# Performance work log

Measured on AMD Instinct MI355X. Metric: run time of the kernel, lower is better.

## Reference

```python
import jax, jax.numpy as jnp
import numpy as np

EMBED = 192
EXPAND = 3
D1 = EMBED * EXPAND  # 576
RPE_IN = 32
LAYERS = 3
LAMBDA = 0.95


def _rpe_mlp(t, w0, b0, ws, bs, wo, bo):
    # t: (2n, 1) relative positions -> (2n, D1) Toeplitz coefficients
    h = t @ w0.T + b0
    for i in range(ws.shape[0]):
        h = jax.nn.relu(h) @ ws[i].T + bs[i]
    return jax.nn.relu(h) @ wo.T + bo


def _toeplitz(x, a):
    # Toeplitz matmul via length-2n circular convolution (FFT).
    # x: (B, n, d); a: (2n, d) coeffs ordered [t0, t1..t_{n-1}, pad, neg half]
    n = x.shape[1]
    m = 2 * n
    xf = jnp.fft.rfft(x, m, axis=1)
    af = jnp.fft.rfft(a, m, axis=0)
    return jnp.fft.irfft(xf * af[None], m, axis=1)[:, :n]


def _forward(x, p_w, p_b, q_w, q_b, v_w, v_b, o_w, o_b, slope,
             t1_w0, t1_b0, t1_ws, t1_bs, t1_wo, t1_bo,
             t2_w0, t2_b0, t2_ws, t2_bs, t2_wo, t2_bo):
    b, h, w, d = x.shape
    n = h  # square grid: h == w, rpe/decay built from n = x.shape[1]
    dt = x.dtype

    pos = jnp.arange(1, n, dtype=dt).reshape(-1, 1)          # (n-1, 1)
    zero = jnp.zeros((1, 1), dt)
    rpe_input = jnp.concatenate([zero, pos, zero, -pos], axis=0)  # (2n, 1)

    p = jax.nn.silu(x @ p_w.T + p_b)
    q = jax.nn.silu(x @ q_w.T + q_b)
    v = jax.nn.silu(x @ v_w.T + v_b)

    # decay mask: slope clamped to [0,1], blended with lambda, powered by |lag|
    sl = LAMBDA + (1.0 - LAMBDA) * jnp.clip(slope, 0.0, 1.0)  # (1, D1)
    idx = jnp.arange(1, n, dtype=dt).reshape(1, -1, 1)        # (1, n-1, 1)
    gamma = sl ** idx                                          # (1, n-1, D1)
    one = jnp.ones((1, 1, D1), dt)
    decay = jnp.concatenate([one, gamma, one, gamma[:, ::-1]], axis=1)[0]  # (2n, D1)

    a1 = _rpe_mlp(rpe_input, t1_w0, t1_b0, t1_ws, t1_bs, t1_wo, t1_bo) * decay
    a2 = _rpe_mlp(rpe_input, t2_w0, t2_b0, t2_ws, t2_bs, t2_wo, t2_bo) * decay

    qv = q * v                                                 # (b, h, w, D1)
    # axial mixing: tno1 along width, tno2 along height
    o1 = _toeplitz(qv.reshape(b * h, w, D1), a1).reshape(b, h, w, D1)
    o2 = _toeplitz(jnp.transpose(qv, (0, 2, 1, 3)).reshape(b * w, h, D1), a2)
    o2 = jnp.transpose(o2.reshape(b, w, h, D1), (0, 2, 1, 3))
    out = p * (o1 + o2)
    return out @ o_w.T + o_b


def setup_inputs() -> dict:
    key = jax.random.key(0)
    ks = jax.random.split(key, 8)

    def lin(k, out_d, in_d):
        k1, k2 = jax.random.split(k)
        s = 1.0 / np.sqrt(in_d)
        return (jax.random.uniform(k1, (out_d, in_d), jnp.float32, -s, s),
                jax.random.uniform(k2, (out_d,), jnp.float32, -s, s))

    x = jax.random.normal(ks[0], (8, 56, 56, EMBED), jnp.float32)
    p_w, p_b = lin(ks[1], D1, EMBED)
    q_w, q_b = lin(ks[2], D1, EMBED)
    v_w, v_b = lin(ks[3], D1, EMBED)
    o_w, o_b = lin(ks[4], EMBED, D1)
    # slope init: 1/arange(1, d1+1)^(1/(index+1)), index=0
    slope = (1.0 / jnp.arange(1, D1 + 1, dtype=jnp.float32)).reshape(1, -1)

    def tno_params(kb):
        kk = jax.random.split(kb, 2 + LAYERS)
        w0, b0 = lin(kk[0], RPE_IN, 1)
        ws, bs = [], []
        for i in range(LAYERS):
            wi, bi = lin(kk[1 + i], RPE_IN, RPE_IN)
            ws.append(wi); bs.append(bi)
        wo, bo = lin(kk[1 + LAYERS], D1, RPE_IN)
        return w0, b0, jnp.stack(ws), jnp.stack(bs), wo, bo

    t1 = tno_params(ks[5])
    t2 = tno_params(ks[6])
    return {"x": x, "p_w": p_w, "p_b": p_b, "q_w": q_w, "q_b": q_b,
            "v_w": v_w, "v_b": v_b, "o_w": o_w, "o_b": o_b, "slope": slope,
            "t1_w0": t1[0], "t1_b0": t1[1], "t1_ws": t1[2], "t1_bs": t1[3], "t1_wo": t1[4], "t1_bo": t1[5],
            "t2_w0": t2[0], "t2_b0": t2[1], "t2_ws": t2[2], "t2_bs": t2[3], "t2_wo": t2[4], "t2_bo": t2[5]}


def reference(x, p_w, p_b, q_w, q_b, v_w, v_b, o_w, o_b, slope,
              t1_w0, t1_b0, t1_ws, t1_bs, t1_wo, t1_bo,
              t2_w0, t2_b0, t2_ws, t2_bs, t2_wo, t2_bo):
    return _forward(x, p_w, p_b, q_w, q_b, v_w, v_b, o_w, o_b, slope,
                    t1_w0, t1_b0, t1_ws, t1_bs, t1_wo, t1_bo,
                    t2_w0, t2_b0, t2_ws, t2_bs, t2_wo, t2_bo)
```

## Files before the change

### kernel.cpp

```cpp
#include <hip/hip_runtime.h>
#include <hip/hip_bf16.h>
#include <math.h>

typedef unsigned short u16;
typedef short bf16x8 __attribute__((ext_vector_type(8)));
typedef float f32x4 __attribute__((ext_vector_type(4)));

#define NB 8
#define NN 56
#define M2 112
#define EMB 192
#define D1 576
#define TOK (NB*NN*NN)

__device__ __forceinline__ float bf2f(unsigned int u) {
    union { unsigned int i; float f; } v; v.i = u << 16; return v.f;
}
__device__ __forceinline__ u16 f2bf(float f) {
    union { float f; unsigned int i; } v; v.f = f;
    unsigned int x = v.i;
    return (u16)((x + 0x7fffu + ((x >> 16) & 1u)) >> 16);
}
__device__ __forceinline__ float fast_silu(float x) {
    float e = __builtin_amdgcn_exp2f(-1.442695041f * x);
    return x * __builtin_amdgcn_rcpf(1.0f + e);
}
__device__ __forceinline__ void async16(void* lds, const void* g) {
    __builtin_amdgcn_global_load_lds(
        (const __attribute__((address_space(1))) void*)g,
        (__attribute__((address_space(3))) void*)lds, 16, 0, 0);
}

#define XCH (TOK*EMB/4)
#define WCH (D1*EMB/4)
__global__ __launch_bounds__(256) void convert_kernel(
    const float* __restrict__ x,
    const float* __restrict__ pw, const float* __restrict__ qw,
    const float* __restrict__ vw, const float* __restrict__ ow,
    u16* __restrict__ xb, u16* __restrict__ wb, u16* __restrict__ owb)
{
    int tid = blockIdx.x * 256 + threadIdx.x;
    const float* src; u16* dst; int off;
    if (tid < XCH) { src = x; dst = xb; off = tid; }
    else {
        int r = tid - XCH;
        int seg = r / WCH; off = r % WCH;
        if (seg == 0)      { src = pw; dst = wb; }
        else if (seg == 1) { src = qw; dst = wb + D1*EMB; }
        else if (seg == 2) { src = vw; dst = wb + 2*D1*EMB; }
        else if (seg == 3) { src = ow; dst = owb; }
        else return;
    }
    float4 f = *(const float4*)(src + off * 4);
    ushort4 o;
    o.x = f2bf(f.x); o.y = f2bf(f.y); o.z = f2bf(f.z); o.w = f2bf(f.w);
    *(ushort4*)(dst + off * 4) = o;
}

__global__ __launch_bounds__(576) void rpe_kernel(
    const float* __restrict__ slope,
    const float* w0a, const float* b0a, const float* wsa, const float* bsa,
    const float* woa, const float* boa,
    const float* w0b, const float* b0b, const float* wsb, const float* bsb,
    const float* wob, const float* bob,
    float* __restrict__ A1, float* __restrict__ A2)
{
    int wq  = blockIdx.x / M2;
    int row = blockIdx.x % M2;
    const float* w0 = wq ? w0b : w0a;  const float* b0 = wq ? b0b : b0a;
    const float* ws = wq ? wsb : wsa;  const float* bs = wq ? bsb : bsa;
    const float* wo = wq ? wob : woa;  const float* bo = wq ? bob : boa;
    float* A = wq ? A2 : A1;

    float tval = (row == 0 || row == 56) ? 0.0f
               : (row < 56 ? (float)row : -(float)(row - 56));
    int kexp = (row == 0 || row == 56) ? 0 : (row < 56 ? row : 112 - row);

    __shared__ float h[32], g[32];
    int t = threadIdx.x;
    if (t < 32) h[t] = tval * w0[t] + b0[t];
    __syncthreads();
    for (int L = 0; L < 3; L++) {
        if (t < 32) g[t] = fmaxf(h[t], 0.0f);
        __syncthreads();
        float hn = 0.0f;
        if (t < 32) {
            hn = bs[L * 32 + t];
            for (int k = 0; k < 32; k++)
                hn = fmaf(g[k], ws[(L * 32 + t) * 32 + k], hn);
        }
        __syncthreads();
        if (t < 32) h[t] = hn;
        __syncthreads();
    }
    if (t < 32) g[t] = fmaxf(h[t], 0.0f);
    __syncthreads();

    float o = bo[t];
    for (int k = 0; k < 32; k++)
        o = fmaf(g[k], wo[t * 32 + k], o);

    float sl = slope[t];
    sl = 0.95f + 0.05f * fminf(fmaxf(sl, 0.0f), 1.0f);
    float dec = powf(sl, (float)kexp);
    A[row * D1 + t] = o * dec;
}

__global__ __launch_bounds__(256) void tbuild_kernel(
    const float* __restrict__ A1, const float* __restrict__ A2,
    u16* __restrict__ T1t, u16* __restrict__ T2t)
{
    int d = blockIdx.x;
    const float* src = blockIdx.y ? A2 : A1;
    u16* dst = blockIdx.y ? T2t : T1t;
    __shared__ float win[111];
    int t = threadIdx.x;
    if (t < 111) {
        int lag = t - 55;
        int rowi = lag + (lag < 0 ? 112 : 0);
        win[t] = src[rowi * D1 + d];
    }
    __syncthreads();
    int i = t >> 2, jq = (t & 3) * 16;
    u16 vals[16];
    #pragma unroll
    for (int jj = 0; jj < 16; jj++) {
        int j = jq + jj;
        float v = (i < 56 && j < 56) ? win[i - j + 55] : 0.0f;
        vals[jj] = f2bf(v);
    }
    u16* out = dst + ((size_t)d * 64 + i) * 64 + jq;
    *(uint4*)(out)     = *(uint4*)&vals[0];
    *(uint4*)(out + 8) = *(uint4*)&vals[8];
}

__global__ __launch_bounds__(512, 4) void proj_kernel(
    const u16* __restrict__ xb, const u16* __restrict__ wb,
    const float* __restrict__ pb, const float* __restrict__ qb,
    const float* __restrict__ vb,
    u16* __restrict__ P_T, u16* __restrict__ QV_T)
{
    __shared__ u16 lds[40960];
    int m0 = blockIdx.x * 128, n0 = blockIdx.y * 64;
    int t = threadIdx.x;
    int l = t & 63, wave = t >> 6;
    int wm = wave >> 2, wn = wave & 3;
    int col16 = l & 15, q = l >> 4;

    f32x4 accp[4], accq[4], accv[4];
    #pragma unroll
    for (int i = 0; i < 4; i++) {
        accp[i] = (f32x4){0,0,0,0};
        accq[i] = (f32x4){0,0,0,0};
        accv[i] = (f32x4){0,0,0,0};
    }

    auto stage = [&](int kc, int buf) {
        int bo = buf * 20480;
        #pragma unroll
        for (int ii = 0; ii < 2; ii++) {
            int slot = ii * 512 + t;
            int r = slot >> 3, s = slot & 7;
            int g = s ^ (r & 7);
            async16(&lds[bo + slot * 8], xb + (m0 + r) * EMB + kc * 64 + g * 8);
        }
        #pragma unroll
        for (int ii = 0; ii < 3; ii++) {
            int slot = ii * 512 + t;
            int mat = slot >> 9, cc = slot & 511;
            int r = cc >> 3, s = cc & 7;
            int g = s ^ (r & 7);
            async16(&lds[bo + 8192 + slot * 8],
                    wb + mat * (D1 * EMB) + (n0 + r) * EMB + kc * 64 + g * 8);
        }
    };

    auto compute = [&](int bo) {
        #pragma unroll
        for (int kk = 0; kk < 2; kk++) {
            int sw = ((q + 4 * kk) ^ (col16 & 7)) * 8;
            bf16x8 af[4];
            #pragma unroll
            for (int mt = 0; mt < 4; mt++)
                af[mt] = *(const bf16x8*)&lds[bo + (wm * 64 + mt * 16 + col16) * 64 + sw];
            bf16x8 bfr[3];
            #pragma unroll
            for (int mat = 0; mat < 3; mat++)
                bfr[mat] = *(const bf16x8*)&lds[bo + 8192 + mat * 4096 + (wn * 16 + col16) * 64 + sw];
            #pragma unroll
            for (int mt = 0; mt < 4; mt++) {
                accp[mt] = __builtin_amdgcn_mfma_f32_16x16x32_bf16(af[mt], bfr[0], accp[mt], 0, 0, 0);
                accq[mt] = __builtin_amdgcn_mfma_f32_16x16x32_bf16(af[mt], bfr[1], accq[mt], 0, 0, 0);
                accv[mt] = __builtin_amdgcn_mfma_f32_16x16x32_bf16(af[mt], bfr[2], accv[mt], 0, 0, 0);
            }
        }
    };

    stage(0, 0);
    stage(1, 1);
    asm volatile("s_waitcnt vmcnt(5)" ::: "memory");
    __builtin_amdgcn_s_barrier();
    compute(0);
    __builtin_amdgcn_s_barrier();
    stage(2, 0);
    asm volatile("s_waitcnt vmcnt(5)" ::: "memory");
    __builtin_amdgcn_s_barrier();
    compute(20480);
    asm volatile("s_waitcnt vmcnt(0)" ::: "memory");
    __builtin_amdgcn_s_barrier();
    compute(0);

    int n = n0 + wn * 16 + col16;
    float pbv = pb[n], qbv = qb[n], vbv = vb[n];
    size_t drow = (size_t)n * TOK + m0 + wm * 64;
    #pragma unroll
    for (int mt = 0; mt < 4; mt++) {
        ushort4 o;
        o.x = f2bf(fast_silu(accp[mt][0] + pbv));
        o.y = f2bf(fast_silu(accp[mt][1] + pbv));
        o.z = f2bf(fast_silu(accp[mt][2] + pbv));
        o.w = f2bf(fast_silu(accp[mt][3] + pbv));
        *(ushort4*)&P_T[drow + mt * 16 + q * 4] = o;
    }
    #pragma unroll
    for (int mt = 0; mt < 4; mt++) {
        ushort4 o;
        o.x = f2bf(fast_silu(accq[mt][0] + qbv) * fast_silu(accv[mt][0] + vbv));
        o.y = f2bf(fast_silu(accq[mt][1] + qbv) * fast_silu(accv[mt][1] + vbv));
        o.z = f2bf(fast_silu(accq[mt][2] + qbv) * fast_silu(accv[mt][2] + vbv));
        o.w = f2bf(fast_silu(accq[mt][3] + qbv) * fast_silu(accv[mt][3] + vbv));
        *(ushort4*)&QV_T[drow + mt * 16 + q * 4] = o;
    }
}

__global__ __launch_bounds__(256) void tno_mfma(
    const u16* __restrict__ QV_T, const u16* __restrict__ T1t,
    const u16* __restrict__ T2t, const u16* __restrict__ P_T,
    u16* __restrict__ U_T)
{
    __shared__ u16 T1s[4096];
    __shared__ u16 T2s[4096];
    __shared__ u16 Qn[64 * 72];
    __shared__ u16 Qt[64 * 72];
    __shared__ float O1f[56 * 68];
    int d = blockIdx.x, b = blockIdx.y;
    int t = threadIdx.x;
    size_t base = (size_t)d * TOK + (size_t)b * 3136;

    #pragma unroll
    for (int k = 0; k < 2; k++) {
        int slot = t + k * 256;
        int i = slot >> 3, s = slot & 7;
        int g = s ^ (i & 7);
        async16(&T1s[slot * 8], T1t + ((size_t)d * 64 + i) * 64 + g * 8);
        async16(&T2s[slot * 8], T2t + ((size_t)d * 64 + i) * 64 + g * 8);
    }
    for (int c = t; c < 392; c += 256) {
        int h = c / 7, w8 = (c % 7) * 8;
        uint4 v = *(const uint4*)(QV_T + base + c * 8);
        *(uint4*)&Qn[h * 72 + w8] = v;
        u16 e[8];
        *(uint4*)e = v;
        #pragma unroll
        for (int k = 0; k < 8; k++)
            Qt[(w8 + k) * 72 + h] = e[k];
    }
    if (t < 56) {
        uint4 z = {0, 0, 0, 0};
        *(uint4*)&Qn[t * 72 + 56] = z;
        *(uint4*)&Qt[t * 72 + 56] = z;
    }
    __syncthreads();

    int l = t & 63, wave = t >> 6;
    int col16 = l & 15, q = l >> 4;

    f32x4 acc1[4], acc2[4];
    #pragma unroll
    for (int i = 0; i < 4; i++) { acc1[i] = (f32x4){0,0,0,0}; acc2[i] = (f32x4){0,0,0,0}; }

    #pragma unroll
    for (int kk = 0; kk < 2; kk++) {
        int sw = ((q + 4 * kk) ^ (col16 & 7)) * 8;
        bf16x8 bq1 = *(const bf16x8*)&Qn[(wave * 16 + col16) * 72 + kk * 32 + q * 8];
        bf16x8 bq2 = *(const bf16x8*)&Qt[(wave * 16 + col16) * 72 + kk * 32 + q * 8];
        #pragma unroll
        for (int mt = 0; mt < 4; mt++) {
            bf16x8 a1 = *(const bf16x8*)&T1s[(mt * 16 + col16) * 64 + sw];
            bf16x8 a2 = *(const bf16x8*)&T2s[(mt * 16 + col16) * 64 + sw];
            acc1[mt] = __builtin_amdgcn_mfma_f32_16x16x32_bf16(a1, bq1, acc1[mt], 0, 0, 0);
            acc2[mt] = __builtin_amdgcn_mfma_f32_16x16x32_bf16(a2, bq2, acc2[mt], 0, 0, 0);
        }
    }

    {
        int n = wave * 16 + col16;
        if (n < 56) {
            #pragma unroll
            for (int mt = 0; mt < 4; mt++)
                #pragma unroll
                for (int r = 0; r < 4; r++) {
                    int m = mt * 16 + q * 4 + r;
                    if (m < 56) O1f[n * 68 + m] = acc1[mt][r];
                }
        }
    }
    __syncthreads();
    {
        int n = wave * 16 + col16;
        if (n < 56) {
            #pragma unroll
            for (int mt = 0; mt < 4; mt++)
                #pragma unroll
                for (int r = 0; r < 4; r++) {
                    int m = mt * 16 + q * 4 + r;
                    if (m < 56) O1f[m * 68 + n] += acc2[mt][r];
                }
        }
    }
    __syncthreads();
    for (int c = t; c < 392; c += 256) {
        int h = c / 7, w8 = (c % 7) * 8;
        f32x4 s0 = *(const f32x4*)&O1f[h * 68 + w8];
        f32x4 s1 = *(const f32x4*)&O1f[h * 68 + w8 + 4];
        uint4 pv = *(const uint4*)(P_T + base + c * 8);
        u16 pe[8];
        *(uint4*)pe = pv;
        u16 ue[8];
        #pragma unroll
        for (int k = 0; k < 4; k++) ue[k] = f2bf(bf2f(pe[k]) * s0[k]);
        #pragma unroll
        for (int k = 0; k < 4; k++) ue[4 + k] = f2bf(bf2f(pe[4 + k]) * s1[k]);
        *(uint4*)(U_T + base + c * 8) = *(uint4*)ue;
    }
}

__global__ __launch_bounds__(256) void outproj_kernel(
    const u16* __restrict__ U_T, const u16* __restrict__ owb,
    const float* __restrict__ ob, float* __restrict__ out)
{
    __shared__ char ldsraw[40960];
    u16* Uscr = (u16*)ldsraw;
    u16* As   = (u16*)(ldsraw + 16384);
    u16* Bs   = (u16*)(ldsraw + 32768);
    int m0 = blockIdx.x * 128, n0 = blockIdx.y * 64;
    int t = threadIdx.x;
    int l = t & 63, wave = t >> 6;
    int wm = wave >> 1, wn = wave & 1;
    int col16 = l & 15, q = l >> 4;

    f32x4 acc[4][2];
    #pragma unroll
    for (int i = 0; i < 4; i++)
        #pragma unroll
        for (int j = 0; j < 2; j++) acc[i][j] = (f32x4){0,0,0,0};

    for (int k0 = 0; k0 < 9; k0++) {
        #pragma unroll
        for (int ii = 0; ii < 4; ii++) {
            int slot = ii * 256 + t;
            int dd = slot >> 4, tk = slot & 15;
            async16(&Uscr[slot * 8],
                    U_T + (size_t)(k0 * 64 + dd) * TOK + m0 + tk * 8);
        }
        #pragma unroll
        for (int ii = 0; ii < 2; ii++) {
            int slot = ii * 256 + t;
            int r = slot >> 3, s = slot & 7;
            int g = s ^ (r & 7);
            async16(&Bs[slot * 8], owb + (n0 + r) * D1 + k0 * 64 + g * 8);
        }
        asm volatile("s_waitcnt vmcnt(2)" ::: "memory");
        __builtin_amdgcn_s_barrier();
        #pragma unroll
        for (int ii = 0; ii < 4; ii++) {
            int c = ii * 256 + t;
            int tok = c & 127, dc = c >> 7;
            u16 e[8];
            #pragma unroll
            for (int j = 0; j < 8; j++)
                e[j] = Uscr[(dc * 8 + j) * 128 + tok];
            int s = dc ^ (tok & 7);
            *(uint4*)&As[tok * 64 + s * 8] = *(uint4*)e;
        }
        __syncthreads();

        #pragma unroll
        for (int kk = 0; kk < 2; kk++) {
            int sw = ((q + 4 * kk) ^ (col16 & 7)) * 8;
            bf16x8 af[4];
            #pragma unroll
            for (int mt = 0; mt < 4; mt++)
                af[mt] = *(const bf16x8*)&As[(wm * 64 + mt * 16 + col16) * 64 + sw];
            bf16x8 bfr[2];
            #pragma unroll
            for (int nt = 0; nt < 2; nt++)
                bfr[nt] = *(const bf16x8*)&Bs[(wn * 32 + nt * 16 + col16) * 64 + sw];
            #pragma unroll
            for (int mt = 0; mt < 4; mt++)
                #pragma unroll
                for (int nt = 0; nt < 2; nt++)
                    acc[mt][nt] = __builtin_amdgcn_mfma_f32_16x16x32_bf16(
                        af[mt], bfr[nt], acc[mt][nt], 0, 0, 0);
        }
        __syncthreads();
    }

    float* scr = (float*)ldsraw + wave * 2304;
    float obv[2];
    #pragma unroll
    for (int nt = 0; nt < 2; nt++)
        obv[nt] = ob[n0 + wn * 32 + nt * 16 + col16];
    #pragma unroll
    for (int mt = 0; mt < 4; mt++)
        #pragma unroll
        for (int nt = 0; nt < 2; nt++)
            #pragma unroll
            for (int r = 0; r < 4; r++)
                scr[(mt * 16 + q * 4 + r) * 36 + nt * 16 + col16] =
                    acc[mt][nt][r] + obv[nt];
    __syncthreads();
    #pragma unroll
    for (int k = 0; k < 8; k++) {
        int row = k * 8 + (l >> 3), cs = (l & 7) * 4;
        f32x4 v = *(const f32x4*)&scr[row * 36 + cs];
        *(f32x4*)&out[(m0 + wm * 64 + row) * EMB + n0 + wn * 32 + cs] = v;
    }
}

extern "C" void kernel_launch(void* const* d_in, const int* in_sizes, int n_in,
                              void* d_out, int out_size, void* d_ws, size_t ws_size,
                              hipStream_t stream)
{
    (void)in_sizes; (void)n_in; (void)out_size; (void)ws_size;
    const float* x     = (const float*)d_in[0];
    const float* p_w   = (const float*)d_in[1];
    const float* p_b   = (const float*)d_in[2];
    const float* q_w   = (const float*)d_in[3];
    const float* q_b   = (const float*)d_in[4];
    const float* v_w   = (const float*)d_in[5];
    const float* v_b   = (const float*)d_in[6];
    const float* o_w   = (const float*)d_in[7];
    const float* o_b   = (const float*)d_in[8];
    const float* slope = (const float*)d_in[9];
    const float* t1_w0 = (const float*)d_in[10];
    const float* t1_b0 = (const float*)d_in[11];
    const float* t1_ws = (const float*)d_in[12];
    const float* t1_bs = (const float*)d_in[13];
    const float* t1_wo = (const float*)d_in[14];
    const float* t1_bo = (const float*)d_in[15];
    const float* t2_w0 = (const float*)d_in[16];
    const float* t2_b0 = (const float*)d_in[17];
    const float* t2_ws = (const float*)d_in[18];
    const float* t2_bs = (const float*)d_in[19];
    const float* t2_wo = (const float*)d_in[20];
    const float* t2_bo = (const float*)d_in[21];

    char* ws = (char*)d_ws;
    float* A1  = (float*)ws;
    float* A2  = (float*)(ws + 258048);
    u16*   PT  = (u16*)(ws + 516096);
    u16*   QVT = (u16*)(ws + 29417472);
    u16*   UT  = (u16*)(ws + 58318848);
    u16*   xb  = (u16*)(ws + 87220224);
    u16*   wb  = (u16*)(ws + 96854016);
    u16*   owb = (u16*)(ws + 97517568);
    u16*   T1t = (u16*)(ws + 97738752);
    u16*   T2t = (u16*)(ws + 102457344);

    convert_kernel<<<(XCH + 4*WCH + 255) / 256, 256, 0, stream>>>(
        x, p_w, q_w, v_w, o_w, xb, wb, owb);
    rpe_kernel<<<224, 576, 0, stream>>>(slope,
        t1_w0, t1_b0, t1_ws, t1_bs, t1_wo, t1_bo,
        t2_w0, t2_b0, t2_ws, t2_bs, t2_wo, t2_bo, A1, A2);
    tbuild_kernel<<<dim3(576, 2), 256, 0, stream>>>(A1, A2, T1t, T2t);
    proj_kernel<<<dim3(TOK / 128, D1 / 64), 512, 0, stream>>>(
        xb, wb, p_b, q_b, v_b, PT, QVT);
    tno_mfma<<<dim3(D1, NB), 256, 0, stream>>>(QVT, T1t, T2t, PT, UT);
    outproj_kernel<<<dim3(TOK / 128, EMB / 64), 256, 0, stream>>>(
        UT, owb, o_b, (float*)d_out);
}
```

Before: 200.8 us.

## Enlarge proj GEMM M tile to 256 and drop LDS double buffering

The projection kernel now covers 256 tokens per block instead of 128. Each wave computes a 64x32 output tile (2 N sub-tiles) instead of 64x16, so every A fragment read from LDS feeds more MFMAs. The two-buffer async pipeline is replaced with a single buffer that is loaded, waited on, and computed for each k-chunk. This cuts LDS footprint and redundant B loads, but it removes the overlap of loads with compute, doubles accumulator registers (which may limit occupancy under launch_bounds 512,4), and halves the grid size.

```diff
diff --git a/kernel.cpp b/kernel.cpp
--- a/kernel.cpp
+++ b/kernel.cpp
@@ -140,96 +140,101 @@
     const float* __restrict__ vb,
     u16* __restrict__ P_T, u16* __restrict__ QV_T)
 {
-    __shared__ u16 lds[40960];
-    int m0 = blockIdx.x * 128, n0 = blockIdx.y * 64;
+    __shared__ u16 lds[28672];
+    u16* As = lds;
+    u16* Bs = lds + 16384;
+    int m0 = blockIdx.x * 256, n0 = blockIdx.y * 64;
     int t = threadIdx.x;
     int l = t & 63, wave = t >> 6;
-    int wm = wave >> 2, wn = wave & 3;
+    int wg = wave >> 1, wn = wave & 1;
     int col16 = l & 15, q = l >> 4;
 
-    f32x4 accp[4], accq[4], accv[4];
-    #pragma unroll
-    for (int i = 0; i < 4; i++) {
-        accp[i] = (f32x4){0,0,0,0};
-        accq[i] = (f32x4){0,0,0,0};
-        accv[i] = (f32x4){0,0,0,0};
-    }
-
-    auto stage = [&](int kc, int buf) {
-        int bo = buf * 20480;
-        #pragma unroll
-        for (int ii = 0; ii < 2; ii++) {
-            int slot = ii * 512 + t;
-            int r = slot >> 3, s = slot & 7;
+    f32x4 accp[4][2], accq[4][2], accv[4][2];
+    #pragma unroll
+    for (int i = 0; i < 4; i++)
+        #pragma unroll
+        for (int j = 0; j < 2; j++) {
+            accp[i][j] = (f32x4){0,0,0,0};
+            accq[i][j] = (f32x4){0,0,0,0};
+            accv[i][j] = (f32x4){0,0,0,0};
+        }
+
+    auto stage = [&](int kc) {
+        #pragma unroll
+        for (int ii = 0; ii < 4; ii++) {
+            int c = ii * 512 + t;
+            int r = c >> 3, s = c & 7;
             int g = s ^ (r & 7);
-            async16(&lds[bo + slot * 8], xb + (m0 + r) * EMB + kc * 64 + g * 8);
+            async16(&As[c * 8], xb + (m0 + r) * EMB + kc * 64 + g * 8);
         }
         #pragma unroll
         for (int ii = 0; ii < 3; ii++) {
-            int slot = ii * 512 + t;
-            int mat = slot >> 9, cc = slot & 511;
+            int c = ii * 512 + t;
+            int mat = c >> 9, cc = c & 511;
             int r = cc >> 3, s = cc & 7;
             int g = s ^ (r & 7);
-            async16(&lds[bo + 8192 + slot * 8],
+            async16(&Bs[c * 8],
                     wb + mat * (D1 * EMB) + (n0 + r) * EMB + kc * 64 + g * 8);
         }
     };
 
-    auto compute = [&](int bo) {
+    #pragma unroll
+    for (int kc = 0; kc < 3; kc++) {
+        stage(kc);
+        asm volatile("s_waitcnt vmcnt(0)" ::: "memory");
+        __builtin_amdgcn_s_barrier();
         #pragma unroll
         for (int kk = 0; kk < 2; kk++) {
             int sw = ((q + 4 * kk) ^ (col16 & 7)) * 8;
             bf16x8 af[4];
             #pragma unroll
             for (int mt = 0; mt < 4; mt++)
-                af[mt] = *(const bf16x8*)&lds[bo + (wm * 64 + mt * 16 + col16) * 64 + sw];
-            bf16x8 bfr[3];
+                af[mt] = *(const bf16x8*)&As[(wg * 64 + mt * 16 + col16) * 64 + sw];
+            bf16x8 bfr[3][2];
             #pragma unroll
             for (int mat = 0; mat < 3; mat++)
-                bfr[mat] = *(const bf16x8*)&lds[bo + 8192 + mat * 4096 + (wn * 16 + col16) * 64 + sw];
-            #pragma unroll
-            for (int mt = 0; mt < 4; mt++) {
-                accp[mt] = __builtin_amdgcn_mfma_f32_16x16x32_bf16(af[mt], bfr[0], accp[mt], 0, 0, 0);
-                accq[mt] = __builtin_amdgcn_mfma_f32_16x16x32_bf16(af[mt], bfr[1], accq[mt], 0, 0, 0);
-                accv[mt] = __builtin_amdgcn_mfma_f32_16x16x32_bf16(af[mt], bfr[2], accv[mt], 0, 0, 0);
-            }
-        }
-    };
-
-    stage(0, 0);
-    stage(1, 1);
-    asm volatile("s_waitcnt vmcnt(5)" ::: "memory");
-    __builtin_amdgcn_s_barrier();
-    compute(0);
-    __builtin_amdgcn_s_barrier();
-    stage(2, 0);
-    asm volatile("s_waitcnt vmcnt(5)" ::: "memory");
-    __builtin_amdgcn_s_barrier();
-    compute(20480);
-    asm volatile("s_waitcnt vmcnt(0)" ::: "memory");
-    __builtin_amdgcn_s_barrier();
-    compute(0);
-
-    int n = n0 + wn * 16 + col16;
-    float pbv = pb[n], qbv = qb[n], vbv = vb[n];
-    size_t drow = (size_t)n * TOK + m0 + wm * 64;
-    #pragma unroll
-    for (int mt = 0; mt < 4; mt++) {
-        ushort4 o;
-        o.x = f2bf(fast_silu(accp[mt][0] + pbv));
-        o.y = f2bf(fast_silu(accp[mt][1] + pbv));
-        o.z = f2bf(fast_silu(accp[mt][2] + pbv));
-        o.w = f2bf(fast_silu(accp[mt][3] + pbv));
-        *(ushort4*)&P_T[drow + mt * 16 + q * 4] = o;
-    }
-    #pragma unroll
-    for (int mt = 0; mt < 4; mt++) {
-        ushort4 o;
-        o.x = f2bf(fast_silu(accq[mt][0] + qbv) * fast_silu(accv[mt][0] + vbv));
-        o.y = f2bf(fast_silu(accq[mt][1] + qbv) * fast_silu(accv[mt][1] + vbv));
-        o.z = f2bf(fast_silu(accq[mt][2] + qbv) * fast_silu(accv[mt][2] + vbv));
-        o.w = f2bf(fast_silu(accq[mt][3] + qbv) * fast_silu(accv[mt][3] + vbv));
-        *(ushort4*)&QV_T[drow + mt * 16 + q * 4] = o;
+                #pragma unroll
+                for (int nt = 0; nt < 2; nt++)
+                    bfr[mat][nt] = *(const bf16x8*)&Bs[mat * 4096 + (wn * 32 + nt * 16 + col16) * 64 + sw];
+            #pragma unroll
+            for (int mt = 0; mt < 4; mt++)
+                #pragma unroll
+                for (int nt = 0; nt < 2; nt++) {
+                    accp[mt][nt] = __builtin_amdgcn_mfma_f32_16x16x32_bf16(af[mt], bfr[0][nt], accp[mt][nt], 0, 0, 0);
+                    accq[mt][nt] = __builtin_amdgcn_mfma_f32_16x16x32_bf16(af[mt], bfr[1][nt], accq[mt][nt], 0, 0, 0);
+                    accv[mt][nt] = __builtin_amdgcn_mfma_f32_16x16x32_bf16(af[mt], bfr[2][nt], accv[mt][nt], 0, 0, 0);
+                }
+        }
+        if (kc < 2) __builtin_amdgcn_s_barrier();
+    }
+
+    float pbv[2], qbv[2], vbv[2];
+    #pragma unroll
+    for (int nt = 0; nt < 2; nt++) {
+        int n = n0 + wn * 32 + nt * 16 + col16;
+        pbv[nt] = pb[n]; qbv[nt] = qb[n]; vbv[nt] = vb[n];
+    }
+    #pragma unroll
+    for (int nt = 0; nt < 2; nt++) {
+        size_t drow = (size_t)(n0 + wn * 32 + nt * 16 + col16) * TOK + m0 + wg * 64;
+        #pragma unroll
+        for (int mt = 0; mt < 4; mt++) {
+            ushort4 o;
+            o.x = f2bf(fast_silu(accp[mt][nt][0] + pbv[nt]));
+            o.y = f2bf(fast_silu(accp[mt][nt][1] + pbv[nt]));
+            o.z = f2bf(fast_silu(accp[mt][nt][2] + pbv[nt]));
+            o.w = f2bf(fast_silu(accp[mt][nt][3] + pbv[nt]));
+            *(ushort4*)&P_T[drow + mt * 16 + q * 4] = o;
+        }
+        #pragma unroll
+        for (int mt = 0; mt < 4; mt++) {
+            ushort4 o;
+            o.x = f2bf(fast_silu(accq[mt][nt][0] + qbv[nt]) * fast_silu(accv[mt][nt][0] + vbv[nt]));
+            o.y = f2bf(fast_silu(accq[mt][nt][1] + qbv[nt]) * fast_silu(accv[mt][nt][1] + vbv[nt]));
+            o.z = f2bf(fast_silu(accq[mt][nt][2] + qbv[nt]) * fast_silu(accv[mt][nt][2] + vbv[nt]));
+            o.w = f2bf(fast_silu(accq[mt][nt][3] + qbv[nt]) * fast_silu(accv[mt][nt][3] + vbv[nt]));
+            *(ushort4*)&QV_T[drow + mt * 16 + q * 4] = o;
+        }
     }
 }
 
@@ -474,7 +479,7 @@
         t1_w0, t1_b0, t1_ws, t1_bs, t1_wo, t1_bo,
         t2_w0, t2_b0, t2_ws, t2_bs, t2_wo, t2_bo, A1, A2);
     tbuild_kernel<<<dim3(576, 2), 256, 0, stream>>>(A1, A2, T1t, T2t);
-    proj_kernel<<<dim3(TOK / 128, D1 / 64), 512, 0, stream>>>(
+    proj_kernel<<<dim3(TOK / 256, D1 / 64), 512, 0, stream>>>(
         xb, wb, p_b, q_b, v_b, PT, QVT);
     tno_mfma<<<dim3(D1, NB), 256, 0, stream>>>(QVT, T1t, T2t, PT, UT);
     outproj_kernel<<<dim3(TOK / 128, EMB / 64), 256, 0, stream>>>(
```

Result: slower. 272.0 us (+35.5%).
